# Kernel optimization log

Hardware: AMD Instinct MI355X
Metric: run time of the kernel (lower is better)

## Reference

```python
import jax, jax.numpy as jnp
import numpy as np

B, L, S, H, E = 2, 2048, 2048, 8, 64
MASK_SCALE = 10000.0
TAU_MIN, TAU_MAX = 0.1, 5.0
THR_MIN, THR_MAX = 0.01, 0.99


def setup_inputs() -> dict:
    key = jax.random.key(0)
    ks = jax.random.split(key, 7)
    query = jax.random.normal(ks[0], (B, L, H, E), jnp.float32)
    k_ = jax.random.normal(ks[1], (B, S, H, E), jnp.float32)
    value = jax.random.normal(ks[2], (B, S, H, E), jnp.float32)
    mask_miss_k = jnp.zeros((B, S), jnp.float32)  # unused in forward
    mask_miss_q = jnp.zeros((B, L), jnp.float32)  # unused in forward
    pos = jnp.arange(B * L, dtype=jnp.int32).reshape(B, L, 1)  # monotone positions per batch
    hard_mask = jax.random.randint(ks[3], (L, S), 0, 2, dtype=jnp.int32)
    hard_mask = hard_mask.at[jnp.arange(L), jnp.arange(S)].set(1)  # keep diagonal open
    # learned parameters / stochastic state
    phi = jax.random.normal(ks[4], (H, L, S), jnp.float32)  # DAG edge logits (per head)
    log_tau_gs = jnp.asarray(np.log(2.0), jnp.float32)
    threshold = jnp.asarray(0.5, jnp.float32)
    u = jax.random.uniform(ks[5], (H, L, S), jnp.float32, 1e-6, 1.0 - 1e-6)  # Gumbel base noise
    return {"query": query, "key": k_, "value": value, "mask_miss_k": mask_miss_k,
            "mask_miss_q": mask_miss_q, "pos": pos, "causal_mask": 1,
            "hard_mask": hard_mask, "phi": phi, "log_tau_gs": log_tau_gs,
            "threshold": threshold, "u": u}


def reference(query, key, value, mask_miss_k, mask_miss_q, pos, causal_mask,
              hard_mask, phi, log_tau_gs, threshold, u):
    e = query.shape[-1]
    scale = 1.0 / np.sqrt(e)
    # scores: (B, H, L, S)
    scores = jnp.einsum('blhe,bshe->bhls', query, key)
    if causal_mask:
        p = pos[..., 0]  # (B, L)
        causal = jnp.where(p[:, None, :] > p[:, :, None], -jnp.inf, 0.0).astype(scores.dtype)
        scores = scores + causal[:, None, :, :]
    # Gumbel-sigmoid relaxed DAG mask
    tau = jnp.clip(jnp.exp(log_tau_gs), TAU_MIN, TAU_MAX)
    gumbel = jnp.log(u + 1e-8) - jnp.log(1.0 - u + 1e-8)
    m_relaxed = jax.nn.sigmoid((gumbel + phi) / tau)  # (H, L, S)
    thr = jnp.clip(threshold, THR_MIN, THR_MAX)
    dag_add = MASK_SCALE * jnp.minimum(m_relaxed - thr, 0.0)  # <=0 additive penalty
    scores = scores + dag_add[None, :, :, :]
    # hard mask applied pre-softmax as -inf
    scores = jnp.where(hard_mask[None, None, :, :] == 0, -jnp.inf, scores)
    att = jax.nn.softmax(scale * scores, axis=-1)  # dropout p=0 (eval)
    out = jnp.einsum('bhls,bshe->blhe', att, value)  # (B, L, H, E)
    return out
```

## Files before the change

kernel.cpp:

```cpp
#include <hip/hip_runtime.h>


#define Bz 2
#define Lz 2048
#define Sz 2048
#define Hz 8
#define Ez 64
#define NSEG 4
#define NEG_BIG (-1e30f)

typedef __attribute__((ext_vector_type(8))) short short8;
typedef __attribute__((ext_vector_type(4))) short short4v;
typedef __attribute__((ext_vector_type(4))) float f32x4;

__device__ __forceinline__ float fast_rcp(float x) { return __builtin_amdgcn_rcpf(x); }

__device__ __forceinline__ short f2bf(float x) {
    unsigned bits = __builtin_bit_cast(unsigned, x);
    bits += 0x7FFFu + ((bits >> 16) & 1u);
    return (short)(bits >> 16);
}

__global__ void pack_qk(const float* __restrict__ q, const float* __restrict__ k,
                        short* __restrict__ qp, short* __restrict__ kp)
{
    const int t = blockIdx.x * 256 + threadIdx.x;
    const float4 qv = ((const float4*)q)[t];
    const float4 kv = ((const float4*)k)[t];
    const int e4   = t & 15;
    const int rest = t >> 4;
    const int h    = rest & 7;
    const int bl   = rest >> 3;
    const int b    = bl >> 11;
    const int l    = bl & 2047;
    const int o    = ((b*Hz + h)*Lz + l)*Ez + e4*4;
    short4v qo, ko;
    qo[0] = f2bf(qv.x*0.125f); qo[1] = f2bf(qv.y*0.125f);
    qo[2] = f2bf(qv.z*0.125f); qo[3] = f2bf(qv.w*0.125f);
    ko[0] = f2bf(kv.x); ko[1] = f2bf(kv.y); ko[2] = f2bf(kv.z); ko[3] = f2bf(kv.w);
    *(short4v*)&qp[o] = qo;
    *(short4v*)&kp[o] = ko;
}

__global__ void pack_vt(const float* __restrict__ v, short* __restrict__ vt)
{
    const int blk = blockIdx.x;
    const int st  = blk & 63;
    const int h   = (blk >> 6) & 7;
    const int b   = blk >> 9;
    const int s0  = st * 32;
    const int e   = threadIdx.x & 63;
    const int sc  = threadIdx.x >> 6;
    short8 ov;
#pragma unroll
    for (int j = 0; j < 8; ++j) {
        const int s = s0 + sc*8 + j;
        ov[j] = f2bf(v[((b*Sz + s)*Hz + h)*Ez + e]);
    }
    *(short8*)&vt[((b*Hz + h)*Ez + e)*Sz + s0 + sc*8] = ov;
}

__global__ __launch_bounds__(256, 2) void attn_main(
    const float* __restrict__ phi, const float* __restrict__ u,
    const int* __restrict__ hard_mask, const int* __restrict__ causal_p,
    const float* __restrict__ log_tau_p, const float* __restrict__ thr_p,
    const short* __restrict__ qp, const short* __restrict__ kp,
    const short* __restrict__ vt,
    float* __restrict__ Op, float* __restrict__ Mp, float* __restrict__ Lp)
{
    const int lane  = threadIdx.x & 63;
    const int wslot = threadIdx.x >> 6;
    const int wu    = blockIdx.x * 4 + wslot;
    const int seg   = wu & 3;
    const int qq    = wu >> 2;
    const int h     = qq & 7;
    const int c     = 127 - (qq >> 3);
    const int l_base = c * 16;
    const int ln    = lane & 15;
    const int quad  = lane >> 4;

    const int causal = *causal_p;
    float tau = __expf(*log_tau_p);
    tau = fminf(fmaxf(tau, 0.1f), 5.0f);
    const float inv_tau = 1.0f / tau;
    const float thr = fminf(fmaxf(*thr_p, 0.01f), 0.99f);

    short8 qf[2][2];
#pragma unroll
    for (int b = 0; b < 2; ++b)
#pragma unroll
        for (int k = 0; k < 2; ++k)
            qf[b][k] = *(const short8*)&qp[((b*Hz + h)*Lz + l_base + ln)*Ez + k*32 + quad*8];

    f32x4 O[2][4];
    float m_r[2][4], l_r[2][4];
#pragma unroll
    for (int b = 0; b < 2; ++b) {
#pragma unroll
        for (int ne = 0; ne < 4; ++ne) { f32x4 z = {0.f,0.f,0.f,0.f}; O[b][ne] = z; }
#pragma unroll
        for (int r = 0; r < 4; ++r) { m_r[b][r] = -INFINITY; l_r[b][r] = 0.f; }
    }

    const int T = causal ? (((l_base + 15) >> 6) + 1) : (Sz >> 6);

    __shared__ __align__(16) short plds[4][16*72];
    short* myp = &plds[wslot][0];

    for (int t = seg; t < T; t += NSEG) {
        const int s0 = t << 6;

        float dg[4][4];
#pragma unroll
        for (int nt = 0; nt < 4; ++nt) {
#pragma unroll
            for (int r = 0; r < 4; ++r) {
                const int l = l_base + quad*4 + r;
                const int s = s0 + nt*16 + ln;
                const int off = (h*Lz + l)*Sz + s;
                const float ph = phi[off];
                const float uv = u[off];
                const int   hm = hard_mask[l*Sz + s];
                const float g  = __logf((uv + 1e-8f) * fast_rcp(1.0f - uv + 1e-8f));
                const float z  = (g + ph) * inv_tau;
                const float sg = fast_rcp(1.0f + __expf(-z));
                const float d  = 1250.0f * fminf(sg - thr, 0.0f);
                const bool dead = (hm == 0) || (causal && (s > l));
                dg[nt][r] = dead ? -INFINITY : d;
            }
        }

#pragma unroll
        for (int b = 0; b < 2; ++b) {
            short8 kf[4][2];
#pragma unroll
            for (int nt = 0; nt < 4; ++nt)
#pragma unroll
                for (int k = 0; k < 2; ++k)
                    kf[nt][k] = *(const short8*)&kp[((b*Hz + h)*Sz + s0 + nt*16 + ln)*Ez + k*32 + quad*8];

            f32x4 Sc[4];
#pragma unroll
            for (int nt = 0; nt < 4; ++nt) {
                f32x4 z4 = {0.f,0.f,0.f,0.f};
                z4 = __builtin_amdgcn_mfma_f32_16x16x32_bf16(qf[b][0], kf[nt][0], z4, 0, 0, 0);
                Sc[nt] = __builtin_amdgcn_mfma_f32_16x16x32_bf16(qf[b][1], kf[nt][1], z4, 0, 0, 0);
            }

            float tv[4][4], mx[4];
#pragma unroll
            for (int r = 0; r < 4; ++r) mx[r] = -INFINITY;
#pragma unroll
            for (int nt = 0; nt < 4; ++nt)
#pragma unroll
                for (int r = 0; r < 4; ++r) {
                    const float val = Sc[nt][r] + dg[nt][r];
                    tv[nt][r] = val;
                    mx[r] = fmaxf(mx[r], val);
                }
#pragma unroll
            for (int r = 0; r < 4; ++r)
#pragma unroll
                for (int o = 1; o < 16; o <<= 1)
                    mx[r] = fmaxf(mx[r], __shfl_xor(mx[r], o, 16));

            float al[4], mn[4];
#pragma unroll
            for (int r = 0; r < 4; ++r) {
                mn[r] = fmaxf(m_r[b][r], mx[r]);
                al[r] = __expf(fmaxf(m_r[b][r], NEG_BIG) - fmaxf(mn[r], NEG_BIG));
                m_r[b][r] = mn[r];
            }

            float ps[4] = {0.f, 0.f, 0.f, 0.f};
#pragma unroll
            for (int nt = 0; nt < 4; ++nt)
#pragma unroll
                for (int r = 0; r < 4; ++r) {
                    const float p = __expf(tv[nt][r] - fmaxf(mn[r], NEG_BIG));
                    ps[r] += p;
                    myp[(quad*4 + r)*72 + nt*16 + ln] = f2bf(p);
                }
#pragma unroll
            for (int r = 0; r < 4; ++r) {
#pragma unroll
                for (int o = 1; o < 16; o <<= 1)
                    ps[r] += __shfl_xor(ps[r], o, 16);
                l_r[b][r] = l_r[b][r] * al[r] + ps[r];
            }
#pragma unroll
            for (int ne = 0; ne < 4; ++ne)
#pragma unroll
                for (int r = 0; r < 4; ++r)
                    O[b][ne][r] *= al[r];

            short8 pa[2];
#pragma unroll
            for (int k = 0; k < 2; ++k)
                pa[k] = *(const short8*)&myp[ln*72 + k*32 + quad*8];

#pragma unroll
            for (int ne = 0; ne < 4; ++ne) {
                const short8 v0 = *(const short8*)&vt[((b*Hz + h)*Ez + ne*16 + ln)*Sz + s0 + quad*8];
                const short8 v1 = *(const short8*)&vt[((b*Hz + h)*Ez + ne*16 + ln)*Sz + s0 + 32 + quad*8];
                O[b][ne] = __builtin_amdgcn_mfma_f32_16x16x32_bf16(pa[0], v0, O[b][ne], 0, 0, 0);
                O[b][ne] = __builtin_amdgcn_mfma_f32_16x16x32_bf16(pa[1], v1, O[b][ne], 0, 0, 0);
            }
        }
    }

#pragma unroll
    for (int b = 0; b < 2; ++b) {
#pragma unroll
        for (int ne = 0; ne < 4; ++ne)
#pragma unroll
            for (int r = 0; r < 4; ++r) {
                const int l = l_base + quad*4 + r;
                Op[(((seg*2 + b)*Hz + h)*Lz + l)*Ez + ne*16 + ln] = O[b][ne][r];
            }
        if (ln == 0) {
#pragma unroll
            for (int r = 0; r < 4; ++r) {
                const int l = l_base + quad*4 + r;
                Mp[((seg*2 + b)*Hz + h)*Lz + l] = m_r[b][r];
                Lp[((seg*2 + b)*Hz + h)*Lz + l] = l_r[b][r];
            }
        }
    }
}

__global__ void merge_k(const float* __restrict__ Op, const float* __restrict__ Mp,
                        const float* __restrict__ Lp, float* __restrict__ out)
{
    const int t = blockIdx.x * 256 + threadIdx.x;
    const int e4   = (t & 15) * 4;
    const int rest = t >> 4;
    const int h    = rest & 7;
    const int bl   = rest >> 3;
    const int b    = bl >> 11;
    const int l    = bl & 2047;

    float ms[NSEG], ls[NSEG], m = -INFINITY;
#pragma unroll
    for (int s = 0; s < NSEG; ++s) {
        const int idx = ((s*2 + b)*Hz + h)*Lz + l;
        ms[s] = Mp[idx];
        ls[s] = Lp[idx];
        m = fmaxf(m, ms[s]);
    }
    const float mg = fmaxf(m, NEG_BIG);
    float den = 0.f, a0 = 0.f, a1 = 0.f, a2 = 0.f, a3 = 0.f;
#pragma unroll
    for (int s = 0; s < NSEG; ++s) {
        const float w = __expf(fmaxf(ms[s], NEG_BIG) - mg);
        den += w * ls[s];
        const float4 ov = *(const float4*)&Op[(((s*2 + b)*Hz + h)*Lz + l)*Ez + e4];
        a0 += w * ov.x; a1 += w * ov.y; a2 += w * ov.z; a3 += w * ov.w;
    }
    const float rd = 1.0f / den;
    float4 res;
    res.x = a0 * rd; res.y = a1 * rd; res.z = a2 * rd; res.w = a3 * rd;
    *(float4*)&out[((b*Lz + l)*Hz + h)*Ez + e4] = res;
}

extern "C" void kernel_launch(void* const* d_in, const int* in_sizes, int n_in,
                              void* d_out, int out_size, void* d_ws, size_t ws_size,
                              hipStream_t stream)
{
    const float* q     = (const float*)d_in[0];
    const float* k     = (const float*)d_in[1];
    const float* v     = (const float*)d_in[2];
    const int*   caus  = (const int*)d_in[6];
    const int*   hm    = (const int*)d_in[7];
    const float* phi   = (const float*)d_in[8];
    const float* ltau  = (const float*)d_in[9];
    const float* thr   = (const float*)d_in[10];
    const float* u     = (const float*)d_in[11];

    char* ws = (char*)d_ws;
    short* qp = (short*)(ws);
    short* kp = (short*)(ws + (size_t)( 4u << 20));
    short* vt = (short*)(ws + (size_t)( 8u << 20));
    float* Op = (float*)(ws + (size_t)(12u << 20));
    float* Mp = (float*)(ws + (size_t)(44u << 20));
    float* Lp = (float*)(ws + (size_t)(44u << 20) + (512u << 10));

    pack_qk <<<2048, 256, 0, stream>>>(q, k, qp, kp);
    pack_vt <<<1024, 256, 0, stream>>>(v, vt);
    attn_main<<<1024, 256, 0, stream>>>(phi, u, hm, caus, ltau, thr, qp, kp, vt, Op, Mp, Lp);
    merge_k <<<2048, 256, 0, stream>>>(Op, Mp, Lp, (float*)d_out);
}
```

Before: 407.9 us.

## Bit-pack hard/causal mask, vectorize phi/u loads with prefetch, stage bias via LDS

The pack kernel now also builds a 64-bit-per-tile dead mask from the hard mask and causal condition. The main kernel uses that mask instead of reading the int32 hard mask, so it fetches far fewer bytes per tile. Phi and u are loaded as float4 rows and prefetched one tile ahead, and the bias is computed in that layout and transposed through LDS into the MFMA layout. Block mapping is simplified so the four waves of a block share one query tile, and launch bounds rise to 3 blocks per SM. This trades extra LDS use and register pressure for fewer, coalesced global loads.

```diff
diff --git a/kernel.cpp b/kernel.cpp
--- a/kernel.cpp
+++ b/kernel.cpp
@@ -8,6 +8,7 @@
 #define Ez 64
 #define NSEG 4
 #define NEG_BIG (-1e30f)
+#define DPAD 68
 
 typedef __attribute__((ext_vector_type(8))) short short8;
 typedef __attribute__((ext_vector_type(4))) short short4v;
@@ -22,7 +23,9 @@
 }
 
 __global__ void pack_qk(const float* __restrict__ q, const float* __restrict__ k,
-                        short* __restrict__ qp, short* __restrict__ kp)
+                        short* __restrict__ qp, short* __restrict__ kp,
+                        const int* __restrict__ hm, const int* __restrict__ caus_p,
+                        unsigned long long* __restrict__ dmask)
 {
     const int t = blockIdx.x * 256 + threadIdx.x;
     const float4 qv = ((const float4*)q)[t];
@@ -40,6 +43,24 @@
     ko[0] = f2bf(kv.x); ko[1] = f2bf(kv.y); ko[2] = f2bf(kv.z); ko[3] = f2bf(kv.w);
     *(short4v*)&qp[o] = qo;
     *(short4v*)&kp[o] = ko;
+
+    if (blockIdx.x < 512) {
+        const int lane = threadIdx.x & 63;
+        const int lrow = blockIdx.x * 4 + (threadIdx.x >> 6);
+        const int causal = *caus_p;
+#pragma unroll 4
+        for (int tt = 0; tt < 32; ++tt) {
+            int dead;
+            if (causal && (tt*64 > lrow)) {
+                dead = 1;
+            } else {
+                const int s = tt*64 + lane;
+                dead = (hm[lrow*Sz + s] == 0) || (causal && (s > lrow));
+            }
+            const unsigned long long m = __ballot(dead);
+            if (lane == 0) dmask[lrow*32 + tt] = m;
+        }
+    }
 }
 
 __global__ void pack_vt(const float* __restrict__ v, short* __restrict__ vt)
@@ -60,9 +81,9 @@
     *(short8*)&vt[((b*Hz + h)*Ez + e)*Sz + s0 + sc*8] = ov;
 }
 
-__global__ __launch_bounds__(256, 2) void attn_main(
+__global__ __launch_bounds__(256, 3) void attn_main(
     const float* __restrict__ phi, const float* __restrict__ u,
-    const int* __restrict__ hard_mask, const int* __restrict__ causal_p,
+    const unsigned long long* __restrict__ dmask, const int* __restrict__ causal_p,
     const float* __restrict__ log_tau_p, const float* __restrict__ thr_p,
     const short* __restrict__ qp, const short* __restrict__ kp,
     const short* __restrict__ vt,
@@ -70,9 +91,8 @@
 {
     const int lane  = threadIdx.x & 63;
     const int wslot = threadIdx.x >> 6;
-    const int wu    = blockIdx.x * 4 + wslot;
-    const int seg   = wu & 3;
-    const int qq    = wu >> 2;
+    const int seg   = wslot;
+    const int qq    = blockIdx.x;
     const int h     = qq & 7;
     const int c     = 127 - (qq >> 3);
     const int l_base = c * 16;
@@ -92,6 +112,15 @@
         for (int k = 0; k < 2; ++k)
             qf[b][k] = *(const short8*)&qp[((b*Hz + h)*Lz + l_base + ln)*Ez + k*32 + quad*8];
 
+    size_t pbase[4];
+    int    mbase[4];
+#pragma unroll
+    for (int i = 0; i < 4; ++i) {
+        const int l = l_base + quad*4 + i;
+        pbase[i] = (size_t)(h*Lz + l)*Sz + (size_t)(ln*4);
+        mbase[i] = l * (Sz/64);
+    }
+
     f32x4 O[2][4];
     float m_r[2][4], l_r[2][4];
 #pragma unroll
@@ -105,30 +134,58 @@
     const int T = causal ? (((l_base + 15) >> 6) + 1) : (Sz >> 6);
 
     __shared__ __align__(16) short plds[4][16*72];
+    __shared__ __align__(16) float dlds[4][16*DPAD];
     short* myp = &plds[wslot][0];
+    float* myd = &dlds[wslot][0];
+
+    f32x4 ph4[4], uu4[4];
+    unsigned long long dm[4];
+    if (seg < T) {
+        const int s0p = seg << 6;
+#pragma unroll
+        for (int i = 0; i < 4; ++i) {
+            ph4[i] = *(const f32x4*)&phi[pbase[i] + s0p];
+            uu4[i] = *(const f32x4*)&u[pbase[i] + s0p];
+            dm[i]  = dmask[mbase[i] + seg];
+        }
+    }
 
     for (int t = seg; t < T; t += NSEG) {
         const int s0 = t << 6;
 
-        float dg[4][4];
-#pragma unroll
-        for (int nt = 0; nt < 4; ++nt) {
-#pragma unroll
-            for (int r = 0; r < 4; ++r) {
-                const int l = l_base + quad*4 + r;
-                const int s = s0 + nt*16 + ln;
-                const int off = (h*Lz + l)*Sz + s;
-                const float ph = phi[off];
-                const float uv = u[off];
-                const int   hm = hard_mask[l*Sz + s];
+#pragma unroll
+        for (int i = 0; i < 4; ++i) {
+            f32x4 dv;
+#pragma unroll
+            for (int j = 0; j < 4; ++j) {
+                const float uv = uu4[i][j];
                 const float g  = __logf((uv + 1e-8f) * fast_rcp(1.0f - uv + 1e-8f));
-                const float z  = (g + ph) * inv_tau;
+                const float z  = (g + ph4[i][j]) * inv_tau;
                 const float sg = fast_rcp(1.0f + __expf(-z));
                 const float d  = 1250.0f * fminf(sg - thr, 0.0f);
-                const bool dead = (hm == 0) || (causal && (s > l));
-                dg[nt][r] = dead ? -INFINITY : d;
-            }
-        }
+                const bool dead = (dm[i] >> (ln*4 + j)) & 1ull;
+                dv[j] = dead ? -INFINITY : d;
+            }
+            *(f32x4*)&myd[(quad*4 + i)*DPAD + ln*4] = dv;
+        }
+
+        const int tn = t + NSEG;
+        if (tn < T) {
+            const int s0n = tn << 6;
+#pragma unroll
+            for (int i = 0; i < 4; ++i) {
+                ph4[i] = *(const f32x4*)&phi[pbase[i] + s0n];
+                uu4[i] = *(const f32x4*)&u[pbase[i] + s0n];
+                dm[i]  = dmask[mbase[i] + tn];
+            }
+        }
+
+        float dg[4][4];
+#pragma unroll
+        for (int nt = 0; nt < 4; ++nt)
+#pragma unroll
+            for (int r = 0; r < 4; ++r)
+                dg[nt][r] = myd[(quad*4 + r)*DPAD + nt*16 + ln];
 
 #pragma unroll
         for (int b = 0; b < 2; ++b) {
@@ -147,16 +204,15 @@
                 Sc[nt] = __builtin_amdgcn_mfma_f32_16x16x32_bf16(qf[b][1], kf[nt][1], z4, 0, 0, 0);
             }
 
-            float tv[4][4], mx[4];
+            float mx[4];
 #pragma unroll
             for (int r = 0; r < 4; ++r) mx[r] = -INFINITY;
 #pragma unroll
             for (int nt = 0; nt < 4; ++nt)
 #pragma unroll
                 for (int r = 0; r < 4; ++r) {
-                    const float val = Sc[nt][r] + dg[nt][r];
-                    tv[nt][r] = val;
-                    mx[r] = fmaxf(mx[r], val);
+                    Sc[nt][r] += dg[nt][r];
+                    mx[r] = fmaxf(mx[r], Sc[nt][r]);
                 }
 #pragma unroll
             for (int r = 0; r < 4; ++r)
@@ -177,7 +233,7 @@
             for (int nt = 0; nt < 4; ++nt)
 #pragma unroll
                 for (int r = 0; r < 4; ++r) {
-                    const float p = __expf(tv[nt][r] - fmaxf(mn[r], NEG_BIG));
+                    const float p = __expf(Sc[nt][r] - fmaxf(mn[r], NEG_BIG));
                     ps[r] += p;
                     myp[(quad*4 + r)*72 + nt*16 + ln] = f2bf(p);
                 }
@@ -284,9 +340,10 @@
     float* Op = (float*)(ws + (size_t)(12u << 20));
     float* Mp = (float*)(ws + (size_t)(44u << 20));
     float* Lp = (float*)(ws + (size_t)(44u << 20) + (512u << 10));
-
-    pack_qk <<<2048, 256, 0, stream>>>(q, k, qp, kp);
+    unsigned long long* dmask = (unsigned long long*)(ws + (size_t)(45u << 20));
+
+    pack_qk <<<2048, 256, 0, stream>>>(q, k, qp, kp, hm, caus, dmask);
     pack_vt <<<1024, 256, 0, stream>>>(v, vt);
-    attn_main<<<1024, 256, 0, stream>>>(phi, u, hm, caus, ltau, thr, qp, kp, vt, Op, Mp, Lp);
+    attn_main<<<1024, 256, 0, stream>>>(phi, u, dmask, caus, ltau, thr, qp, kp, vt, Op, Mp, Lp);
     merge_k <<<2048, 256, 0, stream>>>(Op, Mp, Lp, (float*)d_out);
 }
```

Result: slower. 457.3 us (+12.1%).
